# Performance work log

Measured on AMD Instinct MI355X. Metric: run time of the kernel, lower is better.

Reference implementation:

```python
import jax, jax.numpy as jnp
import numpy as np

B, T, D, H, STRIDE, MLP = 2, 2048, 1024, 16, 8, 4096
HD = D // H
EPS = 1e-5


def _ln(x, g, b):
    m = x.mean(-1, keepdims=True)
    v = x.var(-1, keepdims=True)
    return (x - m) * jax.lax.rsqrt(v + EPS) * g + b


def setup_inputs() -> dict:
    key = jax.random.key(0)
    ks = jax.random.split(key, 6)
    s = lambda k, shape: (jax.random.normal(k, shape, jnp.float32) * 0.02)
    return {
        "x": jax.random.normal(ks[0], (B, T, D), jnp.float32),
        "w_in": s(ks[1], (3 * D, D)),   # torch in_proj_weight
        "b_in": jnp.zeros((3 * D,), jnp.float32),
        "w_out": s(ks[2], (D, D)),      # attn out_proj
        "b_out": jnp.zeros((D,), jnp.float32),
        "w1": s(ks[3], (MLP, D)),       # mlp first Linear (torch layout [out,in])
        "b1": jnp.zeros((MLP,), jnp.float32),
        "w2": s(ks[4], (D, MLP)),       # mlp second Linear
        "b2": jnp.zeros((D,), jnp.float32),
        "ln1_g": jnp.ones((D,), jnp.float32),
        "ln1_b": jnp.zeros((D,), jnp.float32),
        "ln2_g": jnp.ones((D,), jnp.float32),
        "ln2_b": jnp.zeros((D,), jnp.float32),
    }


def reference(x, w_in, b_in, w_out, b_out, w1, b1, w2, b2,
              ln1_g, ln1_b, ln2_g, ln2_b):
    Bs, Ts, Ds = x.shape
    xn = _ln(x, ln1_g, ln1_b)
    # fused qkv projection (torch Linear: y = x @ W.T + b)
    qkv = xn @ w_in.T + b_in                              # [B,T,3D]
    q, k, v = jnp.split(qkv, 3, axis=-1)
    to_heads = lambda t: t.reshape(Bs, Ts, H, HD).transpose(0, 2, 1, 3)
    q, k, v = to_heads(q), to_heads(k), to_heads(v)       # [B,H,T,hd]
    scores = jnp.einsum("bhqd,bhkd->bhqk", q, k) / jnp.sqrt(jnp.float32(HD))
    # mask: rows at multiples of STRIDE attend everywhere; others only to self
    idx = jnp.arange(Ts)
    allowed = ((idx % STRIDE) == 0)[:, None] | (idx[:, None] == idx[None, :])
    scores = jnp.where(allowed, scores, -jnp.inf)
    attn = jax.nn.softmax(scores, axis=-1)
    o = jnp.einsum("bhqk,bhkd->bhqd", attn, v)            # [B,H,T,hd]
    o = o.transpose(0, 2, 1, 3).reshape(Bs, Ts, Ds)
    o = o @ w_out.T + b_out
    x = x + o
    xn = _ln(x, ln2_g, ln2_b)
    h = jax.nn.gelu(xn @ w1.T + b1, approximate=False)    # torch nn.GELU default = exact
    x = x + (h @ w2.T + b2)
    return x
```

## Files before the change

### kernel.cpp

```cpp
#include <hip/hip_runtime.h>

#define D_ 1024
#define T_ 2048
#define B_ 2
#define H_ 16
#define MLP_ 4096
#define NTOK (B_*T_)
#define QG 256
#define L2E 1.44269504088896340736f

typedef float f32x4 __attribute__((ext_vector_type(4)));
typedef __bf16 bf16x8 __attribute__((ext_vector_type(8)));

__device__ __forceinline__ unsigned short f2bf(float f) {
  unsigned int u = __float_as_uint(f);
  u += 0x7fff + ((u >> 16) & 1);
  return (unsigned short)(u >> 16);
}

__device__ __forceinline__ float wave_sum(float v) {
  for (int o = 32; o > 0; o >>= 1) v += __shfl_down(v, o, 64);
  return v;
}

__device__ __forceinline__ void gload16(const unsigned short* g, unsigned short* l) {
  __builtin_amdgcn_global_load_lds(
      (const __attribute__((address_space(1))) void*)g,
      (__attribute__((address_space(3))) void*)l, 16, 0, 0);
}

#define N4_WIN  786432
#define N4_WOUT 262144
#define N4_W1   1048576
#define N4_W2   1048576
__global__ void cast_all_kernel(const float* __restrict__ w_in,
                                const float* __restrict__ w_out,
                                const float* __restrict__ w1,
                                const float* __restrict__ w2,
                                unsigned short* __restrict__ o_in,
                                unsigned short* __restrict__ o_out,
                                unsigned short* __restrict__ o1,
                                unsigned short* __restrict__ o2) {
  int i = blockIdx.x * 256 + threadIdx.x;
  const float* src; unsigned short* dst; int j = i;
  if (i < N4_WIN) { src = w_in; dst = o_in; }
  else if ((j -= N4_WIN) < N4_WOUT) { src = w_out; dst = o_out; }
  else if ((j -= N4_WOUT) < N4_W1) { src = w1; dst = o1; }
  else { j -= N4_W1; src = w2; dst = o2; }
  float4 v = ((const float4*)src)[j];
  ushort4 o;
  o.x = f2bf(v.x); o.y = f2bf(v.y); o.z = f2bf(v.z); o.w = f2bf(v.w);
  ((ushort4*)dst)[j] = o;
}

__global__ void ln_kernel(const float* __restrict__ x, const float* __restrict__ g,
                          const float* __restrict__ b, unsigned short* __restrict__ out) {
  int row = blockIdx.x;
  int tid = threadIdx.x;
  int wave = tid >> 6, lane = tid & 63;
  float4 v = ((const float4*)(x + (size_t)row * D_))[tid];
  float s  = v.x + v.y + v.z + v.w;
  float s2 = v.x*v.x + v.y*v.y + v.z*v.z + v.w*v.w;
  s = wave_sum(s); s2 = wave_sum(s2);
  __shared__ float r1[4], r2[4];
  if (lane == 0) { r1[wave] = s; r2[wave] = s2; }
  __syncthreads();
  float ts  = r1[0] + r1[1] + r1[2] + r1[3];
  float ts2 = r2[0] + r2[1] + r2[2] + r2[3];
  float mean = ts * (1.0f / D_);
  float var  = ts2 * (1.0f / D_) - mean * mean;
  float rs = rsqrtf(var + 1e-5f);
  float4 gv = ((const float4*)g)[tid];
  float4 bv = ((const float4*)b)[tid];
  ushort4 o;
  o.x = f2bf((v.x - mean) * rs * gv.x + bv.x);
  o.y = f2bf((v.y - mean) * rs * gv.y + bv.y);
  o.z = f2bf((v.z - mean) * rs * gv.z + bv.z);
  o.w = f2bf((v.w - mean) * rs * gv.w + bv.w);
  ((ushort4*)(out + (size_t)row * D_))[tid] = o;
}

__global__ void reduce_ln_kernel(const float* __restrict__ part,
                                 const float* __restrict__ x,
                                 const float* __restrict__ bias,
                                 const float* __restrict__ g,
                                 const float* __restrict__ b,
                                 float* __restrict__ x1,
                                 unsigned short* __restrict__ xn2) {
  int row = blockIdx.x;
  int tid = threadIdx.x;
  int wave = tid >> 6, lane = tid & 63;
  size_t base = (size_t)row * (D_ / 4) + tid;
  float4 v = ((const float4*)x)[base];
  float4 bo = ((const float4*)bias)[tid];
  v.x += bo.x; v.y += bo.y; v.z += bo.z; v.w += bo.w;
#pragma unroll
  for (int c = 0; c < 2; ++c) {
    float4 p = ((const float4*)part)[(size_t)c * (NTOK * (D_ / 4)) + base];
    v.x += p.x; v.y += p.y; v.z += p.z; v.w += p.w;
  }
  ((float4*)x1)[base] = v;
  float s  = v.x + v.y + v.z + v.w;
  float s2 = v.x*v.x + v.y*v.y + v.z*v.z + v.w*v.w;
  s = wave_sum(s); s2 = wave_sum(s2);
  __shared__ float r1[4], r2[4];
  if (lane == 0) { r1[wave] = s; r2[wave] = s2; }
  __syncthreads();
  float ts  = r1[0] + r1[1] + r1[2] + r1[3];
  float ts2 = r2[0] + r2[1] + r2[2] + r2[3];
  float mean = ts * (1.0f / D_);
  float var  = ts2 * (1.0f / D_) - mean * mean;
  float rs = rsqrtf(var + 1e-5f);
  float4 gv = ((const float4*)g)[tid];
  float4 bv = ((const float4*)b)[tid];
  ushort4 o;
  o.x = f2bf((v.x - mean) * rs * gv.x + bv.x);
  o.y = f2bf((v.y - mean) * rs * gv.y + bv.y);
  o.z = f2bf((v.z - mean) * rs * gv.z + bv.z);
  o.w = f2bf((v.w - mean) * rs * gv.w + bv.w);
  ((ushort4*)xn2)[base] = o;
}

__global__ void reduce_out_kernel(const float* __restrict__ part,
                                  const float* __restrict__ x1,
                                  const float* __restrict__ bias,
                                  float* __restrict__ out) {
  int i = blockIdx.x * 256 + threadIdx.x;
  float4 v = ((const float4*)x1)[i];
  float4 bo = ((const float4*)bias)[i & (D_ / 4 - 1)];
  v.x += bo.x; v.y += bo.y; v.z += bo.z; v.w += bo.w;
#pragma unroll
  for (int c = 0; c < 4; ++c) {
    float4 p = ((const float4*)part)[(size_t)c * (NTOK * (D_ / 4)) + i];
    v.x += p.x; v.y += p.y; v.z += p.z; v.w += p.w;
  }
  ((float4*)out)[i] = v;
}

template<int EPI, int SWIZ, int LDA, int LDB, int LDC>
__global__ __launch_bounds__(256)
void gemm_kernel(const unsigned short* __restrict__ A, size_t sA,
                 const unsigned short* __restrict__ Bm, size_t sB,
                 void* __restrict__ Cv, size_t sC,
                 const float* __restrict__ bias,
                 unsigned short* __restrict__ aux1,
                 unsigned short* __restrict__ aux2,
                 int K, int nx, int ny, int kshift) {
  __shared__ __align__(16) unsigned short As[128 * 64];
  __shared__ __align__(16) unsigned short Bs[128 * 64];
  const int flat = blockIdx.x;
  int bx, by;
  if (SWIZ == 1) {
    bx = flat / ny; by = flat - bx * ny;
  } else {
    const int sxc = nx >> 1;
    const int nSuper = sxc * (ny >> 2);
    int s = flat % nSuper, pos = flat / nSuper;
    int sx = s % sxc, sy = s / sxc;
    bx = sx * 2 + (pos & 1);
    by = sy * 4 + (pos >> 1);
  }
  const int bz = blockIdx.z;
  const int batch = bz >> kshift;
  const int kOff  = (bz & ((1 << kshift) - 1)) * K;
  const int m0 = by * 128;
  const int n0 = bx * 128;
  const int tid = threadIdx.x;
  const int lane = tid & 63, wave = tid >> 6;
  const int wm = (wave >> 1) * 64, wn = (wave & 1) * 64;
  const int fr = lane & 15, q = lane >> 4;
  const int f0 = ((q)     ^ (fr & 7)) << 3;
  const int f1 = ((4 + q) ^ (fr & 7)) << 3;

  const unsigned short* aP[4];
  const unsigned short* bP[4];
  unsigned short* dA[4];
  unsigned short* dB[4];
#pragma unroll
  for (int p = 0; p < 4; ++p) {
    int l = p * 256 + tid;
    int r = l >> 3;
    int cg = (l & 7) ^ (r & 7);
    aP[p] = A  + (size_t)batch * sA + kOff + (size_t)(m0 + r) * LDA + cg * 8;
    bP[p] = Bm + (size_t)batch * sB + kOff + (size_t)(n0 + r) * LDB + cg * 8;
    dA[p] = &As[l * 8];
    dB[p] = &Bs[l * 8];
  }

  f32x4 acc[4][4] = {};
  for (int ko = 0; ko < K; ko += 64) {
    __syncthreads();
#pragma unroll
    for (int p = 0; p < 4; ++p) {
      gload16(aP[p], dA[p]); gload16(bP[p], dB[p]);
      aP[p] += 64; bP[p] += 64;
    }
    __syncthreads();
    {
      bf16x8 af[4], bfr[4];
#pragma unroll
      for (int i = 0; i < 4; ++i) af[i]  = *(const bf16x8*)&As[(wm + i * 16 + fr) * 64 + f0];
#pragma unroll
      for (int j = 0; j < 4; ++j) bfr[j] = *(const bf16x8*)&Bs[(wn + j * 16 + fr) * 64 + f0];
#pragma unroll
      for (int i = 0; i < 4; ++i)
#pragma unroll
        for (int j = 0; j < 4; ++j)
          acc[i][j] = __builtin_amdgcn_mfma_f32_16x16x32_bf16(af[i], bfr[j], acc[i][j], 0, 0, 0);
    }
    {
      bf16x8 af[4], bfr[4];
#pragma unroll
      for (int i = 0; i < 4; ++i) af[i]  = *(const bf16x8*)&As[(wm + i * 16 + fr) * 64 + f1];
#pragma unroll
      for (int j = 0; j < 4; ++j) bfr[j] = *(const bf16x8*)&Bs[(wn + j * 16 + fr) * 64 + f1];
#pragma unroll
      for (int i = 0; i < 4; ++i)
#pragma unroll
        for (int j = 0; j < 4; ++j)
          acc[i][j] = __builtin_amdgcn_mfma_f32_16x16x32_bf16(af[i], bfr[j], acc[i][j], 0, 0, 0);
    }
  }

  const int col = lane & 15, rbase = (lane >> 4) * 4;
#pragma unroll
  for (int i = 0; i < 4; ++i) {
#pragma unroll
    for (int j = 0; j < 4; ++j) {
      int gn = n0 + wn + j * 16 + col;
      int gmb = m0 + wm + i * 16 + rbase;
      float bv = (EPI == 2 || EPI == 8) ? bias[gn] : 0.0f;
#pragma unroll
      for (int r = 0; r < 4; ++r) {
        int gm = gmb + r;
        float v = acc[i][j][r] + bv;
        if (EPI == 2) {
          float u = v * (1.5957691216f + 0.0713548162f * v * v);
          float gl = v / (1.0f + exp2f(-L2E * u));
          ((unsigned short*)Cv)[(size_t)gm * LDC + gn] = f2bf(gl);
        } else if (EPI == 7) {
          ((float*)Cv)[(size_t)bz * sC + (size_t)gm * LDC + gn] = v;
        } else if (EPI == 8) {
          int sec = gn >> 10;
          int hh = (gn >> 6) & (H_ - 1);
          int dd = gn & 63;
          int t = gm & (T_ - 1);
          int b = gm >> 11;
          unsigned short bf = f2bf(v);
          if (sec == 0) {
            if (!(t & 7))
              aux1[(((size_t)(b * H_ + hh)) * QG + (t >> 3)) * 64 + dd] = bf;
          } else if (sec == 1) {
            aux2[(((size_t)(b * H_ + hh)) * T_ + t) * 64 + dd] = bf;
          } else {
            ((unsigned short*)Cv)[(size_t)gm * D_ + (gn - 2 * D_)] = bf;
          }
        }
      }
    }
  }
}

template<int EPI>
__global__ __launch_bounds__(512)
void gemm256_kernel(const unsigned short* __restrict__ A, int LDA,
                    const unsigned short* __restrict__ Bm, int LDB,
                    void* __restrict__ Cv, size_t sC, int LDC,
                    const float* __restrict__ bias, int K, int nxs) {
  __shared__ __align__(16) unsigned short As[2 * 16384];
  __shared__ __align__(16) unsigned short Bs[2 * 16384];
  const int tid = threadIdx.x;
  const int lane = tid & 63, w = tid >> 6;
  const int wm = w >> 2, wn = w & 3;
  const int fr = lane & 15, q = lane >> 4, xr = fr & 7;

  const int nwg = gridDim.x;
  const int bid = blockIdx.x;
  const int l = (bid & 7) * (nwg >> 3) + (bid >> 3);
  const int bx = l & ((1 << nxs) - 1), by = l >> nxs;
  const int m0 = by * 256, n0 = bx * 256;
  const int kOff = blockIdx.z * K;

  const unsigned short* aS[4];
  const unsigned short* bS[4];
#pragma unroll
  for (int s = 0; s < 4; ++s) {
    int ls = s * 512 + tid;
    int r = ls >> 3;
    int cg = (ls & 7) ^ (r & 7);
    aS[s] = A  + (size_t)(m0 + r) * LDA + kOff + cg * 8;
    bS[s] = Bm + (size_t)(n0 + r) * LDB + kOff + cg * 8;
  }
  const int NT = K >> 6;

#pragma unroll
  for (int s = 0; s < 4; ++s) {
    gload16(aS[s], &As[s * 4096 + tid * 8]);
    gload16(bS[s], &Bs[s * 4096 + tid * 8]);
  }
#pragma unroll
  for (int s = 0; s < 4; ++s) {
    gload16(aS[s] + 64, &As[16384 + s * 4096 + tid * 8]);
    gload16(bS[s] + 64, &Bs[16384 + s * 4096 + tid * 8]);
  }
  asm volatile("s_waitcnt vmcnt(8)");
  __builtin_amdgcn_sched_barrier(0);
  __builtin_amdgcn_s_barrier();
  __builtin_amdgcn_sched_barrier(0);

  const int aOff = ((wm * 128 + fr) << 7) + ((q ^ xr) << 4);
  const int bOff = ((wn * 64 + fr) << 7) + ((q ^ xr) << 4);

  f32x4 acc[8][4] = {};

  for (int t = 0; t < NT; ++t) {
    const int cb = (t & 1) << 15;
    const char* Ab = (const char*)As + cb;
    const char* Bb = (const char*)Bs + cb;
    unsigned short* Ad = (unsigned short*)((char*)As + cb);
    unsigned short* Bd = (unsigned short*)((char*)Bs + cb);
    const int ko2 = (t + 2) << 6;
    bf16x8 af[2][4], bfr[2][4];

#pragma unroll
    for (int i = 0; i < 4; ++i) {
      af[0][i] = *(const bf16x8*)(Ab + aOff + i * 2048);
      af[1][i] = *(const bf16x8*)(Ab + (aOff ^ 64) + i * 2048);
    }
#pragma unroll
    for (int j = 0; j < 2; ++j) {
      bfr[0][j] = *(const bf16x8*)(Bb + bOff + j * 2048);
      bfr[1][j] = *(const bf16x8*)(Bb + (bOff ^ 64) + j * 2048);
    }
    __builtin_amdgcn_sched_barrier(0);
    __builtin_amdgcn_s_barrier();
    __builtin_amdgcn_sched_barrier(0);
    __builtin_amdgcn_s_setprio(1);
#pragma unroll
    for (int i = 0; i < 4; ++i)
#pragma unroll
      for (int j = 0; j < 2; ++j) {
        acc[i][j] = __builtin_amdgcn_mfma_f32_16x16x32_bf16(af[0][i], bfr[0][j], acc[i][j], 0, 0, 0);
        acc[i][j] = __builtin_amdgcn_mfma_f32_16x16x32_bf16(af[1][i], bfr[1][j], acc[i][j], 0, 0, 0);
      }
    __builtin_amdgcn_s_setprio(0);
    __builtin_amdgcn_sched_barrier(0);
    __builtin_amdgcn_s_barrier();
    __builtin_amdgcn_sched_barrier(0);

#pragma unroll
    for (int j = 2; j < 4; ++j) {
      bfr[0][j] = *(const bf16x8*)(Bb + bOff + j * 2048);
      bfr[1][j] = *(const bf16x8*)(Bb + (bOff ^ 64) + j * 2048);
    }
    if (t + 2 < NT) {
      gload16(aS[0] + ko2, Ad + tid * 8);
      gload16(aS[2] + ko2, Ad + 2 * 4096 + tid * 8);
    }
    __builtin_amdgcn_sched_barrier(0);
    __builtin_amdgcn_s_barrier();
    __builtin_amdgcn_sched_barrier(0);
    __builtin_amdgcn_s_setprio(1);
#pragma unroll
    for (int i = 0; i < 4; ++i)
#pragma unroll
      for (int j = 0; j < 2; ++j) {
        acc[i][2 + j] = __builtin_amdgcn_mfma_f32_16x16x32_bf16(af[0][i], bfr[0][2 + j], acc[i][2 + j], 0, 0, 0);
        acc[i][2 + j] = __builtin_amdgcn_mfma_f32_16x16x32_bf16(af[1][i], bfr[1][2 + j], acc[i][2 + j], 0, 0, 0);
      }
    __builtin_amdgcn_s_setprio(0);
    __builtin_amdgcn_sched_barrier(0);
    __builtin_amdgcn_s_barrier();
    __builtin_amdgcn_sched_barrier(0);

#pragma unroll
    for (int i = 0; i < 4; ++i) {
      af[0][i] = *(const bf16x8*)(Ab + (aOff + 8192) + i * 2048);
      af[1][i] = *(const bf16x8*)(Ab + ((aOff + 8192) ^ 64) + i * 2048);
    }
    if (t + 2 < NT) {
      gload16(bS[0] + ko2, Bd + tid * 8);
      gload16(bS[1] + ko2, Bd + 4096 + tid * 8);
      gload16(bS[2] + ko2, Bd + 2 * 4096 + tid * 8);
      gload16(bS[3] + ko2, Bd + 3 * 4096 + tid * 8);
    }
    __builtin_amdgcn_sched_barrier(0);
    __builtin_amdgcn_s_barrier();
    __builtin_amdgcn_sched_barrier(0);
    __builtin_amdgcn_s_setprio(1);
#pragma unroll
    for (int i = 0; i < 4; ++i)
#pragma unroll
      for (int j = 0; j < 2; ++j) {
        acc[4 + i][j] = __builtin_amdgcn_mfma_f32_16x16x32_bf16(af[0][i], bfr[0][j], acc[4 + i][j], 0, 0, 0);
        acc[4 + i][j] = __builtin_amdgcn_mfma_f32_16x16x32_bf16(af[1][i], bfr[1][j], acc[4 + i][j], 0, 0, 0);
      }
    __builtin_amdgcn_s_setprio(0);
    __builtin_amdgcn_sched_barrier(0);
    __builtin_amdgcn_s_barrier();
    __builtin_amdgcn_sched_barrier(0);

    if (t + 2 < NT) {
      gload16(aS[1] + ko2, Ad + 4096 + tid * 8);
      gload16(aS[3] + ko2, Ad + 3 * 4096 + tid * 8);
    }
    if (t + 1 < NT) {
      if (t + 2 < NT) asm volatile("s_waitcnt vmcnt(8)");
      else            asm volatile("s_waitcnt vmcnt(0)");
    }
    __builtin_amdgcn_sched_barrier(0);
    __builtin_amdgcn_s_barrier();
    __builtin_amdgcn_sched_barrier(0);
    __builtin_amdgcn_s_setprio(1);
#pragma unroll
    for (int i = 0; i < 4; ++i)
#pragma unroll
      for (int j = 0; j < 2; ++j) {
        acc[4 + i][2 + j] = __builtin_amdgcn_mfma_f32_16x16x32_bf16(af[0][i], bfr[0][2 + j], acc[4 + i][2 + j], 0, 0, 0);
        acc[4 + i][2 + j] = __builtin_amdgcn_mfma_f32_16x16x32_bf16(af[1][i], bfr[1][2 + j], acc[4 + i][2 + j], 0, 0, 0);
      }
    __builtin_amdgcn_s_setprio(0);
    __builtin_amdgcn_sched_barrier(0);
    __builtin_amdgcn_s_barrier();
    __builtin_amdgcn_sched_barrier(0);
  }

  const int col = lane & 15, rbase = (lane >> 4) * 4;
  const int gm0 = m0 + wm * 128 + rbase;
  const int gn0 = n0 + wn * 64 + col;
#pragma unroll
  for (int mi = 0; mi < 8; ++mi) {
#pragma unroll
    for (int j = 0; j < 4; ++j) {
      int gn = gn0 + j * 16;
      float bv = (EPI == 2) ? bias[gn] : 0.0f;
#pragma unroll
      for (int r = 0; r < 4; ++r) {
        int gm = gm0 + mi * 16 + r;
        float v = acc[mi][j][r] + bv;
        if (EPI == 2) {
          float u = v * (1.5957691216f + 0.0713548162f * v * v);
          float gl = v / (1.0f + exp2f(-L2E * u));
          ((unsigned short*)Cv)[(size_t)gm * LDC + gn] = f2bf(gl);
        } else {
          ((float*)Cv)[(size_t)blockIdx.z * sC + (size_t)gm * LDC + gn] = v;
        }
      }
    }
  }
}

__global__ void vtrans_kernel(const unsigned short* __restrict__ vcomp,
                              unsigned short* __restrict__ Vt) {
  int blk = blockIdx.x;
  int tchunk = blk & 31;
  int bh = blk >> 5;
  int h = bh & (H_ - 1), b = bh >> 4;
  int t0 = tchunk * 64;
  __shared__ unsigned short ls[64][66];
  int tid = threadIdx.x;
#pragma unroll
  for (int it = 0; it < 16; ++it) {
    int linear = it * 256 + tid;
    int d = linear & 63, tl = linear >> 6;
    ls[d][tl] = vcomp[((size_t)(b * T_ + t0 + tl)) * D_ + h * 64 + d];
  }
  __syncthreads();
#pragma unroll
  for (int it = 0; it < 16; ++it) {
    int linear = it * 256 + tid;
    int tl = linear & 63, d = linear >> 6;
    Vt[((size_t)(bh * 64 + d)) * T_ + t0 + tl] = ls[d][tl];
  }
}

__global__ __launch_bounds__(256)
void flash_kernel(const unsigned short* __restrict__ Qg,
                  const unsigned short* __restrict__ Kh,
                  const unsigned short* __restrict__ Vt,
                  float* __restrict__ Opart,
                  float* __restrict__ ml) {
  const int kc = blockIdx.x, qt = blockIdx.y, bh = blockIdx.z;
  const int tid = threadIdx.x;
  const int lane = tid & 63, w = tid >> 6;
  const int fr = lane & 15, quad = lane >> 4;

  __shared__ __align__(16) unsigned short Qs[64 * 64];
  __shared__ __align__(16) unsigned short Ks[128 * 64];
  __shared__ __align__(16) unsigned short Vs[64 * 128];
  __shared__ __align__(16) unsigned short Ps[4 * 16 * 128];

  const unsigned short* Qbase = Qg + ((size_t)bh * 256 + qt * 64) * 64;
#pragma unroll
  for (int p = 0; p < 2; ++p) {
    int linear = p * 256 + tid;
    int r = linear >> 3, c = linear & 7;
    gload16(Qbase + r * 64 + (c ^ (r & 7)) * 8, &Qs[linear * 8]);
  }

  float m_run[4], l_run[4];
  f32x4 O[4] = {};
#pragma unroll
  for (int r = 0; r < 4; ++r) { m_run[r] = -3.0e38f; l_run[r] = 0.f; }

  const unsigned short* Kc = Kh + ((size_t)bh * T_ + kc * 512) * 64;
  const unsigned short* Vc = Vt + (size_t)bh * 64 * T_ + kc * 512;
  unsigned short* Pw = &Ps[w * 2048];
  const int arow = w * 16 + fr;

  for (int kt = 0; kt < 4; ++kt) {
    __syncthreads();
#pragma unroll
    for (int p = 0; p < 4; ++p) {
      int linear = p * 256 + tid;
      int r = linear >> 3, c = linear & 7;
      gload16(Kc + (size_t)(kt * 128 + r) * 64 + (c ^ (r & 7)) * 8, &Ks[linear * 8]);
    }
#pragma unroll
    for (int p = 0; p < 4; ++p) {
      int linear = p * 256 + tid;
      int r = linear >> 4, c = linear & 15;
      gload16(Vc + (size_t)r * T_ + kt * 128 + (c ^ (r & 7)) * 8, &Vs[linear * 8]);
    }
    __syncthreads();

    f32x4 s[8] = {};
    bf16x8 aq[2];
#pragma unroll
    for (int ks = 0; ks < 2; ++ks)
      aq[ks] = *(const bf16x8*)&Qs[arow * 64 + ((ks * 4 + quad) ^ (fr & 7)) * 8];
#pragma unroll
    for (int nf = 0; nf < 8; ++nf) {
      int krow = nf * 16 + fr;
#pragma unroll
      for (int ks = 0; ks < 2; ++ks) {
        bf16x8 bk = *(const bf16x8*)&Ks[krow * 64 + ((ks * 4 + quad) ^ (fr & 7)) * 8];
        s[nf] = __builtin_amdgcn_mfma_f32_16x16x32_bf16(aq[ks], bk, s[nf], 0, 0, 0);
      }
    }
    float alpha[4], rowsum[4];
#pragma unroll
    for (int r = 0; r < 4; ++r) {
      float mt = -3.0e38f;
#pragma unroll
      for (int nf = 0; nf < 8; ++nf) { s[nf][r] *= 0.125f; mt = fmaxf(mt, s[nf][r]); }
#pragma unroll
      for (int x = 1; x < 16; x <<= 1) mt = fmaxf(mt, __shfl_xor(mt, x, 64));
      float mn = fmaxf(m_run[r], mt);
      alpha[r] = exp2f((m_run[r] - mn) * L2E);
      m_run[r] = mn;
      rowsum[r] = 0.f;
    }
#pragma unroll
    for (int nf = 0; nf < 8; ++nf)
#pragma unroll
      for (int r = 0; r < 4; ++r) {
        float p = exp2f((s[nf][r] - m_run[r]) * L2E);
        s[nf][r] = p; rowsum[r] += p;
      }
#pragma unroll
    for (int r = 0; r < 4; ++r) {
#pragma unroll
      for (int x = 1; x < 16; x <<= 1) rowsum[r] += __shfl_xor(rowsum[r], x, 64);
      l_run[r] = l_run[r] * alpha[r] + rowsum[r];
    }
#pragma unroll
    for (int nf = 0; nf < 8; ++nf)
#pragma unroll
      for (int r = 0; r < 4; ++r) {
        int m = quad * 4 + r;
        int c = nf * 2 + (fr >> 3);
        Pw[m * 128 + ((c ^ (m & 7)) * 8) + (fr & 7)] = f2bf(s[nf][r]);
      }
#pragma unroll
    for (int nf2 = 0; nf2 < 4; ++nf2)
#pragma unroll
      for (int r = 0; r < 4; ++r) O[nf2][r] *= alpha[r];
#pragma unroll
    for (int ks2 = 0; ks2 < 4; ++ks2) {
      bf16x8 ap = *(const bf16x8*)&Pw[fr * 128 + (((ks2 * 4 + quad) ^ (fr & 7)) * 8)];
#pragma unroll
      for (int nf2 = 0; nf2 < 4; ++nf2) {
        int vrow = nf2 * 16 + fr;
        bf16x8 bv = *(const bf16x8*)&Vs[vrow * 128 + (((ks2 * 4 + quad) ^ (fr & 7)) * 8)];
        O[nf2] = __builtin_amdgcn_mfma_f32_16x16x32_bf16(ap, bv, O[nf2], 0, 0, 0);
      }
    }
  }

  int qbase = qt * 64 + w * 16;
  float* Ob = Opart + (((size_t)bh * 4 + kc) * 256 + qbase) * 64;
#pragma unroll
  for (int nf2 = 0; nf2 < 4; ++nf2)
#pragma unroll
    for (int r = 0; r < 4; ++r)
      Ob[(size_t)(quad * 4 + r) * 64 + nf2 * 16 + fr] = O[nf2][r];
  if (fr == 0) {
#pragma unroll
    for (int r = 0; r < 4; ++r) {
      size_t mi = ((((size_t)bh * 4 + kc) * 256) + qbase + quad * 4 + r) * 2;
      ml[mi] = m_run[r]; ml[mi + 1] = l_run[r];
    }
  }
}

__global__ void combine_kernel(const float* __restrict__ Opart,
                               const float* __restrict__ ml,
                               unsigned short* __restrict__ vcomp) {
  int idx = blockIdx.x * 256 + threadIdx.x;
  int c = idx & (D_ - 1);
  int qi = (idx >> 10) & (QG - 1);
  int b = idx >> 18;
  int h = c >> 6, d = c & 63;
  int bh = b * H_ + h;
  float m[4], l[4];
  float M = -3.0e38f;
#pragma unroll
  for (int ch = 0; ch < 4; ++ch) {
    size_t r = ((size_t)bh * 4 + ch) * 256 + qi;
    m[ch] = ml[r * 2]; l[ch] = ml[r * 2 + 1];
    M = fmaxf(M, m[ch]);
  }
  float osum = 0.f, lsum = 0.f;
#pragma unroll
  for (int ch = 0; ch < 4; ++ch) {
    size_t r = ((size_t)bh * 4 + ch) * 256 + qi;
    float wgt = exp2f((m[ch] - M) * L2E);
    osum += wgt * Opart[r * 64 + d];
    lsum += wgt * l[ch];
  }
  vcomp[((size_t)(b * T_ + qi * 8)) * D_ + c] = f2bf(osum / lsum);
}

extern "C" void kernel_launch(void* const* d_in, const int* in_sizes, int n_in,
                              void* d_out, int out_size, void* d_ws, size_t ws_size,
                              hipStream_t stream) {
  const float* x     = (const float*)d_in[0];
  const float* w_in  = (const float*)d_in[1];
  const float* b_in  = (const float*)d_in[2];
  const float* w_out = (const float*)d_in[3];
  const float* b_out = (const float*)d_in[4];
  const float* w1    = (const float*)d_in[5];
  const float* b1    = (const float*)d_in[6];
  const float* w2    = (const float*)d_in[7];
  const float* b2    = (const float*)d_in[8];
  const float* ln1_g = (const float*)d_in[9];
  const float* ln1_b = (const float*)d_in[10];
  const float* ln2_g = (const float*)d_in[11];
  const float* ln2_b = (const float*)d_in[12];
  float* out = (float*)d_out;

  char* ws = (char*)d_ws;
  size_t off = 0;
  auto alloc = [&](size_t bytes) -> void* {
    void* p = ws + off;
    off += (bytes + 255) & ~(size_t)255;
    return p;
  };
  unsigned short* w_inb = (unsigned short*)alloc((size_t)3 * D_ * D_ * 2);
  unsigned short* w_outb= (unsigned short*)alloc((size_t)D_ * D_ * 2);
  unsigned short* w1b   = (unsigned short*)alloc((size_t)MLP_ * D_ * 2);
  unsigned short* w2b   = (unsigned short*)alloc((size_t)D_ * MLP_ * 2);
  unsigned short* vcomp = (unsigned short*)alloc((size_t)NTOK * D_ * 2);
  float*          x1    = (float*)         alloc((size_t)NTOK * D_ * 4);
  unsigned short* xn2   = (unsigned short*)alloc((size_t)NTOK * D_ * 2);
  unsigned short* h     = (unsigned short*)alloc((size_t)NTOK * MLP_ * 2);
  char* U = (char*)alloc((size_t)4 * NTOK * D_ * 4);
  float*          P2    = (float*)U;
  unsigned short* xn    = (unsigned short*)U;
  unsigned short* Qg    = (unsigned short*)(U + 8388608);
  unsigned short* Kh    = (unsigned short*)(U + 12582912);
  unsigned short* Vt    = (unsigned short*)(U + 20971520);
  float*          Opart = (float*)         (U + 29360128);
  float*          mlbuf = (float*)         (U + 37748736);

  cast_all_kernel<<<(N4_WIN + N4_WOUT + N4_W1 + N4_W2) / 256, 256, 0, stream>>>(
      w_in, w_out, w1, w2, w_inb, w_outb, w1b, w2b);

  ln_kernel<<<NTOK, 256, 0, stream>>>(x, ln1_g, ln1_b, xn);

  gemm_kernel<8, 2, D_, D_, 3 * D_><<<dim3(24 * 32, 1, 1), 256, 0, stream>>>(
      xn, 0, w_inb, 0, vcomp, 0, b_in, Qg, Kh, D_, 24, 32, 0);

  vtrans_kernel<<<1024, 256, 0, stream>>>(vcomp, Vt);

  flash_kernel<<<dim3(4, 4, 32), 256, 0, stream>>>(Qg, Kh, Vt, Opart, mlbuf);

  combine_kernel<<<2048, 256, 0, stream>>>(Opart, mlbuf, vcomp);

  gemm_kernel<7, 1, D_, D_, D_><<<dim3(8 * 32, 1, 2), 256, 0, stream>>>(
      vcomp, 0, w_outb, 0, P2, (size_t)NTOK * D_, nullptr, nullptr, nullptr,
      512, 8, 32, 1);

  reduce_ln_kernel<<<NTOK, 256, 0, stream>>>(P2, x, b_out, ln2_g, ln2_b, x1, xn2);

  gemm256_kernel<2><<<dim3(256, 1, 1), 512, 0, stream>>>(
      xn2, D_, w1b, D_, h, 0, MLP_, b1, D_, 4);

  gemm256_kernel<7><<<dim3(64, 1, 4), 512, 0, stream>>>(
      h, MLP_, w2b, MLP_, P2, (size_t)NTOK * D_, D_, nullptr, 1024, 2);

  reduce_out_kernel<<<4096, 256, 0, stream>>>(P2, x1, b2, out);
}
```

Baseline: 332.5 us.

## Route QKV and out-proj GEMMs through the pipelined 256x256 GEMM kernel

Removes the simple 128x128 single-buffered GEMM and generalises the double-buffered, barrier-scheduled 256x256 kernel to take arbitrary nx, bias and the QKV scatter epilogue. The QKV projection now runs on 192 large tiles. The out-projection uses 4-way split-K with K=256 and 64 tiles, so reduce_ln now sums four partials instead of two. This aims to get better data reuse and load/compute overlap, at the cost of fewer workgroups, which may leave the QKV and out-proj launches under-occupying the GPU, plus extra partial-sum traffic.

```diff
diff --git a/kernel.cpp b/kernel.cpp
--- a/kernel.cpp
+++ b/kernel.cpp
@@ -95,7 +95,7 @@
   float4 bo = ((const float4*)bias)[tid];
   v.x += bo.x; v.y += bo.y; v.z += bo.z; v.w += bo.w;
 #pragma unroll
-  for (int c = 0; c < 2; ++c) {
+  for (int c = 0; c < 4; ++c) {
     float4 p = ((const float4*)part)[(size_t)c * (NTOK * (D_ / 4)) + base];
     v.x += p.x; v.y += p.y; v.z += p.z; v.w += p.w;
   }
@@ -137,110 +137,193 @@
   ((float4*)out)[i] = v;
 }
 
-template<int EPI, int SWIZ, int LDA, int LDB, int LDC>
-__global__ __launch_bounds__(256)
-void gemm_kernel(const unsigned short* __restrict__ A, size_t sA,
-                 const unsigned short* __restrict__ Bm, size_t sB,
-                 void* __restrict__ Cv, size_t sC,
-                 const float* __restrict__ bias,
-                 unsigned short* __restrict__ aux1,
-                 unsigned short* __restrict__ aux2,
-                 int K, int nx, int ny, int kshift) {
-  __shared__ __align__(16) unsigned short As[128 * 64];
-  __shared__ __align__(16) unsigned short Bs[128 * 64];
-  const int flat = blockIdx.x;
-  int bx, by;
-  if (SWIZ == 1) {
-    bx = flat / ny; by = flat - bx * ny;
-  } else {
-    const int sxc = nx >> 1;
-    const int nSuper = sxc * (ny >> 2);
-    int s = flat % nSuper, pos = flat / nSuper;
-    int sx = s % sxc, sy = s / sxc;
-    bx = sx * 2 + (pos & 1);
-    by = sy * 4 + (pos >> 1);
-  }
-  const int bz = blockIdx.z;
-  const int batch = bz >> kshift;
-  const int kOff  = (bz & ((1 << kshift) - 1)) * K;
-  const int m0 = by * 128;
-  const int n0 = bx * 128;
+template<int EPI>
+__global__ __launch_bounds__(512)
+void gemm256_kernel(const unsigned short* __restrict__ A, int LDA,
+                    const unsigned short* __restrict__ Bm, int LDB,
+                    void* __restrict__ Cv, size_t sC, int LDC,
+                    const float* __restrict__ bias,
+                    unsigned short* __restrict__ aux1,
+                    unsigned short* __restrict__ aux2,
+                    int K, int nx) {
+  __shared__ __align__(16) unsigned short As[2 * 16384];
+  __shared__ __align__(16) unsigned short Bs[2 * 16384];
   const int tid = threadIdx.x;
-  const int lane = tid & 63, wave = tid >> 6;
-  const int wm = (wave >> 1) * 64, wn = (wave & 1) * 64;
-  const int fr = lane & 15, q = lane >> 4;
-  const int f0 = ((q)     ^ (fr & 7)) << 3;
-  const int f1 = ((4 + q) ^ (fr & 7)) << 3;
-
-  const unsigned short* aP[4];
-  const unsigned short* bP[4];
-  unsigned short* dA[4];
-  unsigned short* dB[4];
-#pragma unroll
-  for (int p = 0; p < 4; ++p) {
-    int l = p * 256 + tid;
-    int r = l >> 3;
-    int cg = (l & 7) ^ (r & 7);
-    aP[p] = A  + (size_t)batch * sA + kOff + (size_t)(m0 + r) * LDA + cg * 8;
-    bP[p] = Bm + (size_t)batch * sB + kOff + (size_t)(n0 + r) * LDB + cg * 8;
-    dA[p] = &As[l * 8];
-    dB[p] = &Bs[l * 8];
-  }
-
-  f32x4 acc[4][4] = {};
-  for (int ko = 0; ko < K; ko += 64) {
-    __syncthreads();
-#pragma unroll
-    for (int p = 0; p < 4; ++p) {
-      gload16(aP[p], dA[p]); gload16(bP[p], dB[p]);
-      aP[p] += 64; bP[p] += 64;
-    }
-    __syncthreads();
-    {
-      bf16x8 af[4], bfr[4];
-#pragma unroll
-      for (int i = 0; i < 4; ++i) af[i]  = *(const bf16x8*)&As[(wm + i * 16 + fr) * 64 + f0];
-#pragma unroll
-      for (int j = 0; j < 4; ++j) bfr[j] = *(const bf16x8*)&Bs[(wn + j * 16 + fr) * 64 + f0];
-#pragma unroll
-      for (int i = 0; i < 4; ++i)
-#pragma unroll
-        for (int j = 0; j < 4; ++j)
-          acc[i][j] = __builtin_amdgcn_mfma_f32_16x16x32_bf16(af[i], bfr[j], acc[i][j], 0, 0, 0);
-    }
-    {
-      bf16x8 af[4], bfr[4];
-#pragma unroll
-      for (int i = 0; i < 4; ++i) af[i]  = *(const bf16x8*)&As[(wm + i * 16 + fr) * 64 + f1];
-#pragma unroll
-      for (int j = 0; j < 4; ++j) bfr[j] = *(const bf16x8*)&Bs[(wn + j * 16 + fr) * 64 + f1];
-#pragma unroll
-      for (int i = 0; i < 4; ++i)
-#pragma unroll
-        for (int j = 0; j < 4; ++j)
-          acc[i][j] = __builtin_amdgcn_mfma_f32_16x16x32_bf16(af[i], bfr[j], acc[i][j], 0, 0, 0);
-    }
+  const int lane = tid & 63, w = tid >> 6;
+  const int wm = w >> 2, wn = w & 3;
+  const int fr = lane & 15, q = lane >> 4, xr = fr & 7;
+
+  const int nwg = gridDim.x;
+  const int bid = blockIdx.x;
+  const int l = (bid & 7) * (nwg >> 3) + (bid >> 3);
+  const int bx = l % nx, by = l / nx;
+  const int m0 = by * 256, n0 = bx * 256;
+  const int kOff = blockIdx.z * K;
+
+  const unsigned short* aS[4];
+  const unsigned short* bS[4];
+#pragma unroll
+  for (int s = 0; s < 4; ++s) {
+    int ls = s * 512 + tid;
+    int r = ls >> 3;
+    int cg = (ls & 7) ^ (r & 7);
+    aS[s] = A  + (size_t)(m0 + r) * LDA + kOff + cg * 8;
+    bS[s] = Bm + (size_t)(n0 + r) * LDB + kOff + cg * 8;
+  }
+  const int NT = K >> 6;
+
+#pragma unroll
+  for (int s = 0; s < 4; ++s) {
+    gload16(aS[s], &As[s * 4096 + tid * 8]);
+    gload16(bS[s], &Bs[s * 4096 + tid * 8]);
+  }
+#pragma unroll
+  for (int s = 0; s < 4; ++s) {
+    gload16(aS[s] + 64, &As[16384 + s * 4096 + tid * 8]);
+    gload16(bS[s] + 64, &Bs[16384 + s * 4096 + tid * 8]);
+  }
+  asm volatile("s_waitcnt vmcnt(8)");
+  __builtin_amdgcn_sched_barrier(0);
+  __builtin_amdgcn_s_barrier();
+  __builtin_amdgcn_sched_barrier(0);
+
+  const int aOff = ((wm * 128 + fr) << 7) + ((q ^ xr) << 4);
+  const int bOff = ((wn * 64 + fr) << 7) + ((q ^ xr) << 4);
+
+  f32x4 acc[8][4] = {};
+
+  for (int t = 0; t < NT; ++t) {
+    const int cb = (t & 1) << 15;
+    const char* Ab = (const char*)As + cb;
+    const char* Bb = (const char*)Bs + cb;
+    unsigned short* Ad = (unsigned short*)((char*)As + cb);
+    unsigned short* Bd = (unsigned short*)((char*)Bs + cb);
+    const int ko2 = (t + 2) << 6;
+    bf16x8 af[2][4], bfr[2][4];
+
+#pragma unroll
+    for (int i = 0; i < 4; ++i) {
+      af[0][i] = *(const bf16x8*)(Ab + aOff + i * 2048);
+      af[1][i] = *(const bf16x8*)(Ab + (aOff ^ 64) + i * 2048);
+    }
+#pragma unroll
+    for (int j = 0; j < 2; ++j) {
+      bfr[0][j] = *(const bf16x8*)(Bb + bOff + j * 2048);
+      bfr[1][j] = *(const bf16x8*)(Bb + (bOff ^ 64) + j * 2048);
+    }
+    __builtin_amdgcn_sched_barrier(0);
+    __builtin_amdgcn_s_barrier();
+    __builtin_amdgcn_sched_barrier(0);
+    __builtin_amdgcn_s_setprio(1);
+#pragma unroll
+    for (int i = 0; i < 4; ++i)
+#pragma unroll
+      for (int j = 0; j < 2; ++j) {
+        acc[i][j] = __builtin_amdgcn_mfma_f32_16x16x32_bf16(af[0][i], bfr[0][j], acc[i][j], 0, 0, 0);
+        acc[i][j] = __builtin_amdgcn_mfma_f32_16x16x32_bf16(af[1][i], bfr[1][j], acc[i][j], 0, 0, 0);
+      }
+    __builtin_amdgcn_s_setprio(0);
+    __builtin_amdgcn_sched_barrier(0);
+    __builtin_amdgcn_s_barrier();
+    __builtin_amdgcn_sched_barrier(0);
+
+#pragma unroll
+    for (int j = 2; j < 4; ++j) {
+      bfr[0][j] = *(const bf16x8*)(Bb + bOff + j * 2048);
+      bfr[1][j] = *(const bf16x8*)(Bb + (bOff ^ 64) + j * 2048);
+    }
+    if (t + 2 < NT) {
+      gload16(aS[0] + ko2, Ad + tid * 8);
+      gload16(aS[2] + ko2, Ad + 2 * 4096 + tid * 8);
+    }
+    __builtin_amdgcn_sched_barrier(0);
+    __builtin_amdgcn_s_barrier();
+    __builtin_amdgcn_sched_barrier(0);
+    __builtin_amdgcn_s_setprio(1);
+#pragma unroll
+    for (int i = 0; i < 4; ++i)
+#pragma unroll
+      for (int j = 0; j < 2; ++j) {
+        acc[i][2 + j] = __builtin_amdgcn_mfma_f32_16x16x32_bf16(af[0][i], bfr[0][2 + j], acc[i][2 + j], 0, 0, 0);
+        acc[i][2 + j] = __builtin_amdgcn_mfma_f32_16x16x32_bf16(af[1][i], bfr[1][2 + j], acc[i][2 + j], 0, 0, 0);
+      }
+    __builtin_amdgcn_s_setprio(0);
+    __builtin_amdgcn_sched_barrier(0);
+    __builtin_amdgcn_s_barrier();
+    __builtin_amdgcn_sched_barrier(0);
+
+#pragma unroll
+    for (int i = 0; i < 4; ++i) {
+      af[0][i] = *(const bf16x8*)(Ab + (aOff + 8192) + i * 2048);
+      af[1][i] = *(const bf16x8*)(Ab + ((aOff + 8192) ^ 64) + i * 2048);
+    }
+    if (t + 2 < NT) {
+      gload16(bS[0] + ko2, Bd + tid * 8);
+      gload16(bS[1] + ko2, Bd + 4096 + tid * 8);
+      gload16(bS[2] + ko2, Bd + 2 * 4096 + tid * 8);
+      gload16(bS[3] + ko2, Bd + 3 * 4096 + tid * 8);
+    }
+    __builtin_amdgcn_sched_barrier(0);
+    __builtin_amdgcn_s_barrier();
+    __builtin_amdgcn_sched_barrier(0);
+    __builtin_amdgcn_s_setprio(1);
+#pragma unroll
+    for (int i = 0; i < 4; ++i)
+#pragma unroll
+      for (int j = 0; j < 2; ++j) {
+        acc[4 + i][j] = __builtin_amdgcn_mfma_f32_16x16x32_bf16(af[0][i], bfr[0][j], acc[4 + i][j], 0, 0, 0);
+        acc[4 + i][j] = __builtin_amdgcn_mfma_f32_16x16x32_bf16(af[1][i], bfr[1][j], acc[4 + i][j], 0, 0, 0);
+      }
+    __builtin_amdgcn_s_setprio(0);
+    __builtin_amdgcn_sched_barrier(0);
+    __builtin_amdgcn_s_barrier();
+    __builtin_amdgcn_sched_barrier(0);
+
+    if (t + 2 < NT) {
+      gload16(aS[1] + ko2, Ad + 4096 + tid * 8);
+      gload16(aS[3] + ko2, Ad + 3 * 4096 + tid * 8);
+    }
+    if (t + 1 < NT) {
+      if (t + 2 < NT) asm volatile("s_waitcnt vmcnt(8)");
+      else            asm volatile("s_waitcnt vmcnt(0)");
+    }
+    __builtin_amdgcn_sched_barrier(0);
+    __builtin_amdgcn_s_barrier();
+    __builtin_amdgcn_sched_barrier(0);
+    __builtin_amdgcn_s_setprio(1);
+#pragma unroll
+    for (int i = 0; i < 4; ++i)
+#pragma unroll
+      for (int j = 0; j < 2; ++j) {
+        acc[4 + i][2 + j] = __builtin_amdgcn_mfma_f32_16x16x32_bf16(af[0][i], bfr[0][2 + j], acc[4 + i][2 + j], 0, 0, 0);
+        acc[4 + i][2 + j] = __builtin_amdgcn_mfma_f32_16x16x32_bf16(af[1][i], bfr[1][2 + j], acc[4 + i][2 + j], 0, 0, 0);
+      }
+    __builtin_amdgcn_s_setprio(0);
+    __builtin_amdgcn_sched_barrier(0);
+    __builtin_amdgcn_s_barrier();
+    __builtin_amdgcn_sched_barrier(0);
   }
 
   const int col = lane & 15, rbase = (lane >> 4) * 4;
-#pragma unroll
-  for (int i = 0; i < 4; ++i) {
+  const int gm0 = m0 + wm * 128 + rbase;
+  const int gn0 = n0 + wn * 64 + col;
+#pragma unroll
+  for (int mi = 0; mi < 8; ++mi) {
 #pragma unroll
     for (int j = 0; j < 4; ++j) {
-      int gn = n0 + wn + j * 16 + col;
-      int gmb = m0 + wm + i * 16 + rbase;
+      int gn = gn0 + j * 16;
       float bv = (EPI == 2 || EPI == 8) ? bias[gn] : 0.0f;
 #pragma unroll
       for (int r = 0; r < 4; ++r) {
-        int gm = gmb + r;
-        float v = acc[i][j][r] + bv;
+        int gm = gm0 + mi * 16 + r;
+        float v = acc[mi][j][r] + bv;
         if (EPI == 2) {
           float u = v * (1.5957691216f + 0.0713548162f * v * v);
           float gl = v / (1.0f + exp2f(-L2E * u));
           ((unsigned short*)Cv)[(size_t)gm * LDC + gn] = f2bf(gl);
         } else if (EPI == 7) {
-          ((float*)Cv)[(size_t)bz * sC + (size_t)gm * LDC + gn] = v;
-        } else if (EPI == 8) {
+          ((float*)Cv)[(size_t)blockIdx.z * sC + (size_t)gm * LDC + gn] = v;
+        } else {
           int sec = gn >> 10;
           int hh = (gn >> 6) & (H_ - 1);
           int dd = gn & 63;
@@ -255,195 +338,6 @@
           } else {
             ((unsigned short*)Cv)[(size_t)gm * D_ + (gn - 2 * D_)] = bf;
           }
-        }
-      }
-    }
-  }
-}
-
-template<int EPI>
-__global__ __launch_bounds__(512)
-void gemm256_kernel(const unsigned short* __restrict__ A, int LDA,
-                    const unsigned short* __restrict__ Bm, int LDB,
-                    void* __restrict__ Cv, size_t sC, int LDC,
-                    const float* __restrict__ bias, int K, int nxs) {
-  __shared__ __align__(16) unsigned short As[2 * 16384];
-  __shared__ __align__(16) unsigned short Bs[2 * 16384];
-  const int tid = threadIdx.x;
-  const int lane = tid & 63, w = tid >> 6;
-  const int wm = w >> 2, wn = w & 3;
-  const int fr = lane & 15, q = lane >> 4, xr = fr & 7;
-
-  const int nwg = gridDim.x;
-  const int bid = blockIdx.x;
-  const int l = (bid & 7) * (nwg >> 3) + (bid >> 3);
-  const int bx = l & ((1 << nxs) - 1), by = l >> nxs;
-  const int m0 = by * 256, n0 = bx * 256;
-  const int kOff = blockIdx.z * K;
-
-  const unsigned short* aS[4];
-  const unsigned short* bS[4];
-#pragma unroll
-  for (int s = 0; s < 4; ++s) {
-    int ls = s * 512 + tid;
-    int r = ls >> 3;
-    int cg = (ls & 7) ^ (r & 7);
-    aS[s] = A  + (size_t)(m0 + r) * LDA + kOff + cg * 8;
-    bS[s] = Bm + (size_t)(n0 + r) * LDB + kOff + cg * 8;
-  }
-  const int NT = K >> 6;
-
-#pragma unroll
-  for (int s = 0; s < 4; ++s) {
-    gload16(aS[s], &As[s * 4096 + tid * 8]);
-    gload16(bS[s], &Bs[s * 4096 + tid * 8]);
-  }
-#pragma unroll
-  for (int s = 0; s < 4; ++s) {
-    gload16(aS[s] + 64, &As[16384 + s * 4096 + tid * 8]);
-    gload16(bS[s] + 64, &Bs[16384 + s * 4096 + tid * 8]);
-  }
-  asm volatile("s_waitcnt vmcnt(8)");
-  __builtin_amdgcn_sched_barrier(0);
-  __builtin_amdgcn_s_barrier();
-  __builtin_amdgcn_sched_barrier(0);
-
-  const int aOff = ((wm * 128 + fr) << 7) + ((q ^ xr) << 4);
-  const int bOff = ((wn * 64 + fr) << 7) + ((q ^ xr) << 4);
-
-  f32x4 acc[8][4] = {};
-
-  for (int t = 0; t < NT; ++t) {
-    const int cb = (t & 1) << 15;
-    const char* Ab = (const char*)As + cb;
-    const char* Bb = (const char*)Bs + cb;
-    unsigned short* Ad = (unsigned short*)((char*)As + cb);
-    unsigned short* Bd = (unsigned short*)((char*)Bs + cb);
-    const int ko2 = (t + 2) << 6;
-    bf16x8 af[2][4], bfr[2][4];
-
-#pragma unroll
-    for (int i = 0; i < 4; ++i) {
-      af[0][i] = *(const bf16x8*)(Ab + aOff + i * 2048);
-      af[1][i] = *(const bf16x8*)(Ab + (aOff ^ 64) + i * 2048);
-    }
-#pragma unroll
-    for (int j = 0; j < 2; ++j) {
-      bfr[0][j] = *(const bf16x8*)(Bb + bOff + j * 2048);
-      bfr[1][j] = *(const bf16x8*)(Bb + (bOff ^ 64) + j * 2048);
-    }
-    __builtin_amdgcn_sched_barrier(0);
-    __builtin_amdgcn_s_barrier();
-    __builtin_amdgcn_sched_barrier(0);
-    __builtin_amdgcn_s_setprio(1);
-#pragma unroll
-    for (int i = 0; i < 4; ++i)
-#pragma unroll
-      for (int j = 0; j < 2; ++j) {
-        acc[i][j] = __builtin_amdgcn_mfma_f32_16x16x32_bf16(af[0][i], bfr[0][j], acc[i][j], 0, 0, 0);
-        acc[i][j] = __builtin_amdgcn_mfma_f32_16x16x32_bf16(af[1][i], bfr[1][j], acc[i][j], 0, 0, 0);
-      }
-    __builtin_amdgcn_s_setprio(0);
-    __builtin_amdgcn_sched_barrier(0);
-    __builtin_amdgcn_s_barrier();
-    __builtin_amdgcn_sched_barrier(0);
-
-#pragma unroll
-    for (int j = 2; j < 4; ++j) {
-      bfr[0][j] = *(const bf16x8*)(Bb + bOff + j * 2048);
-      bfr[1][j] = *(const bf16x8*)(Bb + (bOff ^ 64) + j * 2048);
-    }
-    if (t + 2 < NT) {
-      gload16(aS[0] + ko2, Ad + tid * 8);
-      gload16(aS[2] + ko2, Ad + 2 * 4096 + tid * 8);
-    }
-    __builtin_amdgcn_sched_barrier(0);
-    __builtin_amdgcn_s_barrier();
-    __builtin_amdgcn_sched_barrier(0);
-    __builtin_amdgcn_s_setprio(1);
-#pragma unroll
-    for (int i = 0; i < 4; ++i)
-#pragma unroll
-      for (int j = 0; j < 2; ++j) {
-        acc[i][2 + j] = __builtin_amdgcn_mfma_f32_16x16x32_bf16(af[0][i], bfr[0][2 + j], acc[i][2 + j], 0, 0, 0);
-        acc[i][2 + j] = __builtin_amdgcn_mfma_f32_16x16x32_bf16(af[1][i], bfr[1][2 + j], acc[i][2 + j], 0, 0, 0);
-      }
-    __builtin_amdgcn_s_setprio(0);
-    __builtin_amdgcn_sched_barrier(0);
-    __builtin_amdgcn_s_barrier();
-    __builtin_amdgcn_sched_barrier(0);
-
-#pragma unroll
-    for (int i = 0; i < 4; ++i) {
-      af[0][i] = *(const bf16x8*)(Ab + (aOff + 8192) + i * 2048);
-      af[1][i] = *(const bf16x8*)(Ab + ((aOff + 8192) ^ 64) + i * 2048);
-    }
-    if (t + 2 < NT) {
-      gload16(bS[0] + ko2, Bd + tid * 8);
-      gload16(bS[1] + ko2, Bd + 4096 + tid * 8);
-      gload16(bS[2] + ko2, Bd + 2 * 4096 + tid * 8);
-      gload16(bS[3] + ko2, Bd + 3 * 4096 + tid * 8);
-    }
-    __builtin_amdgcn_sched_barrier(0);
-    __builtin_amdgcn_s_barrier();
-    __builtin_amdgcn_sched_barrier(0);
-    __builtin_amdgcn_s_setprio(1);
-#pragma unroll
-    for (int i = 0; i < 4; ++i)
-#pragma unroll
-      for (int j = 0; j < 2; ++j) {
-        acc[4 + i][j] = __builtin_amdgcn_mfma_f32_16x16x32_bf16(af[0][i], bfr[0][j], acc[4 + i][j], 0, 0, 0);
-        acc[4 + i][j] = __builtin_amdgcn_mfma_f32_16x16x32_bf16(af[1][i], bfr[1][j], acc[4 + i][j], 0, 0, 0);
-      }
-    __builtin_amdgcn_s_setprio(0);
-    __builtin_amdgcn_sched_barrier(0);
-    __builtin_amdgcn_s_barrier();
-    __builtin_amdgcn_sched_barrier(0);
-
-    if (t + 2 < NT) {
-      gload16(aS[1] + ko2, Ad + 4096 + tid * 8);
-      gload16(aS[3] + ko2, Ad + 3 * 4096 + tid * 8);
-    }
-    if (t + 1 < NT) {
-      if (t + 2 < NT) asm volatile("s_waitcnt vmcnt(8)");
-      else            asm volatile("s_waitcnt vmcnt(0)");
-    }
-    __builtin_amdgcn_sched_barrier(0);
-    __builtin_amdgcn_s_barrier();
-    __builtin_amdgcn_sched_barrier(0);
-    __builtin_amdgcn_s_setprio(1);
-#pragma unroll
-    for (int i = 0; i < 4; ++i)
-#pragma unroll
-      for (int j = 0; j < 2; ++j) {
-        acc[4 + i][2 + j] = __builtin_amdgcn_mfma_f32_16x16x32_bf16(af[0][i], bfr[0][2 + j], acc[4 + i][2 + j], 0, 0, 0);
-        acc[4 + i][2 + j] = __builtin_amdgcn_mfma_f32_16x16x32_bf16(af[1][i], bfr[1][2 + j], acc[4 + i][2 + j], 0, 0, 0);
-      }
-    __builtin_amdgcn_s_setprio(0);
-    __builtin_amdgcn_sched_barrier(0);
-    __builtin_amdgcn_s_barrier();
-    __builtin_amdgcn_sched_barrier(0);
-  }
-
-  const int col = lane & 15, rbase = (lane >> 4) * 4;
-  const int gm0 = m0 + wm * 128 + rbase;
-  const int gn0 = n0 + wn * 64 + col;
-#pragma unroll
-  for (int mi = 0; mi < 8; ++mi) {
-#pragma unroll
-    for (int j = 0; j < 4; ++j) {
-      int gn = gn0 + j * 16;
-      float bv = (EPI == 2) ? bias[gn] : 0.0f;
-#pragma unroll
-      for (int r = 0; r < 4; ++r) {
-        int gm = gm0 + mi * 16 + r;
-        float v = acc[mi][j][r] + bv;
-        if (EPI == 2) {
-          float u = v * (1.5957691216f + 0.0713548162f * v * v);
-          float gl = v / (1.0f + exp2f(-L2E * u));
-          ((unsigned short*)Cv)[(size_t)gm * LDC + gn] = f2bf(gl);
-        } else {
-          ((float*)Cv)[(size_t)blockIdx.z * sC + (size_t)gm * LDC + gn] = v;
         }
       }
     }
@@ -679,8 +573,8 @@
 
   ln_kernel<<<NTOK, 256, 0, stream>>>(x, ln1_g, ln1_b, xn);
 
-  gemm_kernel<8, 2, D_, D_, 3 * D_><<<dim3(24 * 32, 1, 1), 256, 0, stream>>>(
-      xn, 0, w_inb, 0, vcomp, 0, b_in, Qg, Kh, D_, 24, 32, 0);
+  gemm256_kernel<8><<<dim3(192, 1, 1), 512, 0, stream>>>(
+      xn, D_, w_inb, D_, vcomp, 0, 3 * D_, b_in, Qg, Kh, D_, 12);
 
   vtrans_kernel<<<1024, 256, 0, stream>>>(vcomp, Vt);
 
@@ -688,17 +582,18 @@
 
   combine_kernel<<<2048, 256, 0, stream>>>(Opart, mlbuf, vcomp);
 
-  gemm_kernel<7, 1, D_, D_, D_><<<dim3(8 * 32, 1, 2), 256, 0, stream>>>(
-      vcomp, 0, w_outb, 0, P2, (size_t)NTOK * D_, nullptr, nullptr, nullptr,
-      512, 8, 32, 1);
+  gemm256_kernel<7><<<dim3(64, 1, 4), 512, 0, stream>>>(
+      vcomp, D_, w_outb, D_, P2, (size_t)NTOK * D_, D_, nullptr, nullptr, nullptr,
+      256, 4);
 
   reduce_ln_kernel<<<NTOK, 256, 0, stream>>>(P2, x, b_out, ln2_g, ln2_b, x1, xn2);
 
   gemm256_kernel<2><<<dim3(256, 1, 1), 512, 0, stream>>>(
-      xn2, D_, w1b, D_, h, 0, MLP_, b1, D_, 4);
+      xn2, D_, w1b, D_, h, 0, MLP_, b1, nullptr, nullptr, D_, 16);
 
   gemm256_kernel<7><<<dim3(64, 1, 4), 512, 0, stream>>>(
-      h, MLP_, w2b, MLP_, P2, (size_t)NTOK * D_, D_, nullptr, 1024, 2);
+      h, MLP_, w2b, MLP_, P2, (size_t)NTOK * D_, D_, nullptr, nullptr, nullptr,
+      1024, 4);
 
   reduce_out_kernel<<<4096, 256, 0, stream>>>(P2, x1, b2, out);
 }
```

New measurement: 334.0 us. Within noise of the previous version (+0.5%).
